# Kernel optimization log

Hardware: AMD Instinct MI355X
Metric: run time of the kernel (lower is better)

Reference implementation:

```python
import jax, jax.numpy as jnp
import numpy as np

N_TYPES = 4
N_RELS = 8
N, E, IN_DIM, OUT_DIM = 100000, 1600000, 64, 64
SQRT_DK = float(np.sqrt(OUT_DIM))  # num_heads = 1 -> d_k = out_dim


def setup_inputs() -> dict:
    key = jax.random.key(0)
    ks = jax.random.split(key, 12)
    s = 0.05  # keep activations well-scaled (xavier-ish)
    h = jax.random.normal(ks[0], (N, IN_DIM), jnp.float32)
    node_type = jax.random.randint(ks[1], (N,), 0, N_TYPES, jnp.int32)
    src = jax.random.randint(ks[2], (E,), 0, N, jnp.int32)
    dst = jax.random.randint(ks[3], (E,), 0, N, jnp.int32)
    etype = jax.random.randint(ks[4], (E,), 0, N_RELS, jnp.int32)
    k_lin = jax.random.normal(ks[5], (N_TYPES, IN_DIM, OUT_DIM), jnp.float32) * s
    q_lin = jax.random.normal(ks[6], (N_TYPES, IN_DIM, OUT_DIM), jnp.float32) * s
    v_lin = jax.random.normal(ks[7], (N_TYPES, IN_DIM, OUT_DIM), jnp.float32) * s
    a_lin = jax.random.normal(ks[8], (N_TYPES, OUT_DIM, OUT_DIM), jnp.float32) * s
    rel_att = jax.random.normal(ks[9], (N_RELS, OUT_DIM, OUT_DIM), jnp.float32) * s
    rel_msg = jax.random.normal(ks[10], (N_RELS, OUT_DIM, OUT_DIM), jnp.float32) * s
    rel_pri = jnp.ones((N_RELS,), jnp.float32)
    skip = jnp.ones((N_TYPES,), jnp.float32)
    return dict(h=h, node_type=node_type, src=src, dst=dst, etype=etype,
                k_lin=k_lin, q_lin=q_lin, v_lin=v_lin, a_lin=a_lin,
                rel_att=rel_att, rel_msg=rel_msg, rel_pri=rel_pri, skip=skip)


def _typed_matmul(x, W, node_type):
    # rgnn_relational_matmul_no_scatter_gather_list: per-node-type GEMM.
    # Small fixed loop over node types (4), masked accumulate.
    out = jnp.zeros((x.shape[0], W.shape[-1]), x.dtype)
    for t in range(W.shape[0]):
        out = out + jnp.where((node_type == t)[:, None], x @ W[t], 0.0)
    return out


def reference(h, node_type, src, dst, etype, k_lin, q_lin, v_lin, a_lin,
              rel_att, rel_msg, rel_pri, skip):
    # per-node-type K/Q/V projections (num_heads==1, d_k==out_dim)
    k = _typed_matmul(h, k_lin, node_type)  # [N, d_k]
    q = _typed_matmul(h, q_lin, node_type)  # [N, d_k]
    v = _typed_matmul(h, v_lin, node_type)  # [N, d_k]

    # q @ relation_att, computed per relation for ALL nodes then gathered per edge
    # (avoids materializing [E, d_k, d_k] relation weights per edge)
    qW = jnp.einsum('nd,rde->rne', q, rel_att)  # [R, N, d_k]
    t_edge = qW[etype, dst]                      # [E, d_k]  (dst-side product)
    # attention score: <q_dst @ W_att_r, k_src>
    score = jnp.sum(t_edge * k[src], axis=-1)    # [E]

    # edge softmax over incoming edges of each dst, scaled by pri/sqrt(d_k)
    logits = score * (rel_pri / SQRT_DK)[etype]
    m = jax.ops.segment_max(logits, dst, num_segments=N)
    ex = jnp.exp(logits - m[dst])
    den = jax.ops.segment_sum(ex, dst, num_segments=N)
    alpha = ex / jnp.where(den[dst] == 0, 1.0, den[dst])  # [E]

    # message: v_src @ W_msg_r, per relation then gathered per edge
    vW = jnp.einsum('nd,rde->rne', v, rel_msg)   # [R, N, d_k]
    msg = vW[etype, src]                          # [E, d_k]

    # softmax-weighted aggregation to dst nodes
    agg = jax.ops.segment_sum(alpha[:, None] * msg, dst, num_segments=N)  # [N, d_k]

    # output per-node-type GEMM with sigmoid(skip)-scaled a_linears
    W_out = jax.nn.sigmoid(skip)[:, None, None] * a_lin
    return _typed_matmul(agg, W_out, node_type)  # [N, out_dim]
```

## Files before the change

kernel.cpp:

```cpp
#include <hip/hip_runtime.h>
#include <math.h>

#define DIM 64
#define NT 4
#define NR 8

typedef __attribute__((ext_vector_type(8))) short bf16x8;
typedef __attribute__((ext_vector_type(8))) unsigned short u16x8;
typedef __attribute__((ext_vector_type(4))) float f32x4;

__device__ __forceinline__ unsigned short f2bf(float f) {
    unsigned u = __float_as_uint(f);
    return (unsigned short)((u + 0x7FFF + ((u >> 16) & 1)) >> 16);
}
__device__ __forceinline__ float bf2f(unsigned short u) {
    return __uint_as_float((unsigned)u << 16);
}
__device__ __forceinline__ bf16x8 ldb16(const unsigned short* p) {
    return *((const bf16x8*)p);
}

__global__ void prep_all(const float* __restrict__ A, const float* __restrict__ Mw,
                         const float* __restrict__ kl, const float* __restrict__ ql,
                         const float* __restrict__ vl,
                         unsigned short* __restrict__ At, unsigned short* __restrict__ Mt,
                         unsigned short* __restrict__ Wkt, unsigned short* __restrict__ Wqt,
                         unsigned short* __restrict__ Wvt,
                         int* __restrict__ cnt8, int* __restrict__ tm, int M) {
    int i = blockIdx.x * blockDim.x + threadIdx.x;
    if (i < M) cnt8[i] = 0;
    if (i < 16) tm[i] = 0;
    if (i >= 28 * DIM * DIM) return;
    int mat = i >> 12;
    int idx = i & 4095;
    int n = idx >> 6;
    int k = idx & 63;
    int so = k * DIM + n;
    if (mat < 8)       At [((size_t)mat << 12) + idx]        = f2bf(A [((size_t)mat << 12) + so]);
    else if (mat < 16) Mt [((size_t)(mat - 8) << 12) + idx]  = f2bf(Mw[((size_t)(mat - 8) << 12) + so]);
    else if (mat < 20) Wkt[((size_t)(mat - 16) << 12) + idx] = f2bf(kl[((size_t)(mat - 16) << 12) + so]);
    else if (mat < 24) Wqt[((size_t)(mat - 20) << 12) + idx] = f2bf(ql[((size_t)(mat - 20) << 12) + so]);
    else               Wvt[((size_t)(mat - 24) << 12) + idx] = f2bf(vl[((size_t)(mat - 24) << 12) + so]);
}

__global__ void type_count(const int* __restrict__ ntype, int* __restrict__ tm,
                           int* __restrict__ order, int N, int ocap) {
    int i = blockIdx.x * blockDim.x + threadIdx.x;
    if (i < ocap) order[i] = -1;
    int t = (i < N) ? ntype[i] : -1;
    int lane = threadIdx.x & 63;
    #pragma unroll
    for (int tt = 0; tt < NT; tt++) {
        unsigned long long m = __ballot(t == tt);
        int c = __popcll(m);
        if (c && lane == (__ffsll((long long)m) - 1)) atomicAdd(&tm[tt], c);
    }
}

__global__ void type_scan(int* __restrict__ tm) {
    if (threadIdx.x == 0 && blockIdx.x == 0) {
        int b = 0;
        for (int t = 0; t < NT; t++) { tm[4 + t] = b; b += ((tm[t] + 63) >> 6) << 6; }
        tm[12] = b;
    }
}

__global__ void type_scatter(const int* __restrict__ ntype, int* __restrict__ tm,
                             int* __restrict__ order, int N) {
    int i = blockIdx.x * blockDim.x + threadIdx.x;
    int t = (i < N) ? ntype[i] : -1;
    int lane = threadIdx.x & 63;
    #pragma unroll
    for (int tt = 0; tt < NT; tt++) {
        unsigned long long m = __ballot(t == tt);
        int c = __popcll(m);
        if (!c) continue;
        int ldr = __ffsll((long long)m) - 1;
        int base = 0;
        if (lane == ldr) base = atomicAdd(&tm[8 + tt], c);
        base = __shfl(base, ldr, 64);
        if (t == tt) {
            int rank = __popcll(m & ((1ull << lane) - 1ull));
            order[tm[4 + tt] + base + rank] = i;
        }
    }
}

__global__ void __launch_bounds__(256)
proj_mfma(const float* __restrict__ h, const int* __restrict__ ntype,
          const int* __restrict__ order, const int* __restrict__ tm,
          const unsigned short* __restrict__ Wkt, const unsigned short* __restrict__ Wqt,
          const unsigned short* __restrict__ Wvt,
          unsigned short* __restrict__ kvbf, unsigned short* __restrict__ qbf, int N) {
    __shared__ __align__(16) unsigned short xs[64][72];
    int t  = threadIdx.x;
    int n0 = blockIdx.x * 64;
    if (n0 >= tm[12]) return;
    int first = order[n0];
    if (first < 0) return;
    int ty = ntype[first];

    int grow[2];
    #pragma unroll
    for (int i = 0; i < 2; i++) grow[i] = order[n0 + (t + 256 * i) / 8];

    #pragma unroll
    for (int i = 0; i < 4; i++) {
        int idx = t + 256 * i;
        int row = idx >> 4, c4 = idx & 15;
        int gn = order[n0 + row];
        float4 xv = make_float4(0.f, 0.f, 0.f, 0.f);
        if (gn >= 0) xv = ((const float4*)(h + (size_t)gn * DIM))[c4];
        ushort4 b = make_ushort4(f2bf(xv.x), f2bf(xv.y), f2bf(xv.z), f2bf(xv.w));
        *((ushort4*)&xs[row][c4 * 4]) = b;
    }
    __syncthreads();

    int wave = t >> 6, lane = t & 63;
    int m = lane & 15, quad = lane >> 4;
    bf16x8 xa0 = *((const bf16x8*)&xs[wave * 16 + m][quad * 8]);
    bf16x8 xa1 = *((const bf16x8*)&xs[wave * 16 + m][32 + quad * 8]);

    const unsigned short* Wt[3] = { Wkt + (size_t)ty * 4096,
                                    Wqt + (size_t)ty * 4096,
                                    Wvt + (size_t)ty * 4096 };
    for (int mm = 0; mm < 3; mm++) {
        const unsigned short* W = Wt[mm];
        f32x4 c0 = {0.f,0.f,0.f,0.f}, c1 = c0, c2 = c0, c3 = c0;
        c0 = __builtin_amdgcn_mfma_f32_16x16x32_bf16(xa0, ldb16(W + (( 0 + m) << 6)      + quad * 8), c0, 0, 0, 0);
        c1 = __builtin_amdgcn_mfma_f32_16x16x32_bf16(xa0, ldb16(W + ((16 + m) << 6)      + quad * 8), c1, 0, 0, 0);
        c2 = __builtin_amdgcn_mfma_f32_16x16x32_bf16(xa0, ldb16(W + ((32 + m) << 6)      + quad * 8), c2, 0, 0, 0);
        c3 = __builtin_amdgcn_mfma_f32_16x16x32_bf16(xa0, ldb16(W + ((48 + m) << 6)      + quad * 8), c3, 0, 0, 0);
        c0 = __builtin_amdgcn_mfma_f32_16x16x32_bf16(xa1, ldb16(W + (( 0 + m) << 6) + 32 + quad * 8), c0, 0, 0, 0);
        c1 = __builtin_amdgcn_mfma_f32_16x16x32_bf16(xa1, ldb16(W + ((16 + m) << 6) + 32 + quad * 8), c1, 0, 0, 0);
        c2 = __builtin_amdgcn_mfma_f32_16x16x32_bf16(xa1, ldb16(W + ((32 + m) << 6) + 32 + quad * 8), c2, 0, 0, 0);
        c3 = __builtin_amdgcn_mfma_f32_16x16x32_bf16(xa1, ldb16(W + ((48 + m) << 6) + 32 + quad * 8), c3, 0, 0, 0);

        __syncthreads();
        #pragma unroll
        for (int reg = 0; reg < 4; reg++) {
            unsigned short* qr = &xs[wave * 16 + quad * 4 + reg][m];
            qr[ 0] = f2bf(c0[reg]); qr[16] = f2bf(c1[reg]);
            qr[32] = f2bf(c2[reg]); qr[48] = f2bf(c3[reg]);
        }
        __syncthreads();
        #pragma unroll
        for (int i = 0; i < 2; i++) {
            int idx = t + 256 * i;
            int row = idx >> 3, c8 = idx & 7;
            u16x8 v = *((const u16x8*)&xs[row][c8 * 8]);
            if (mm == 1) {
                *((u16x8*)(qbf + ((size_t)(n0 + row) << 6) + c8 * 8)) = v;
            } else {
                int gn = grow[i];
                if (gn >= 0) {
                    unsigned short* dp = (mm == 0)
                        ? kvbf + ((size_t)gn << 7) + c8 * 8
                        : kvbf + ((size_t)gn << 7) + 64 + c8 * 8;
                    *((u16x8*)dp) = v;
                }
            }
        }
    }
}

__global__ void hist8(const int* __restrict__ dst, const int* __restrict__ et,
                      int* __restrict__ cnt, int* __restrict__ rank, int E) {
    int e = blockIdx.x * blockDim.x + threadIdx.x;
    if (e < E) rank[e] = atomicAdd(&cnt[dst[e] * NR + et[e]], 1);
}

__global__ void scan1(const int* __restrict__ cnt, int* __restrict__ off,
                      int* __restrict__ bsum, int M) {
    __shared__ int wsum[16];
    int tid = threadIdx.x;
    int lane = tid & 63, wid = tid >> 6;
    int i = blockIdx.x * 1024 + tid;
    int x0 = (i < M) ? cnt[i] : 0;
    int x = x0;
    #pragma unroll
    for (int s = 1; s < 64; s <<= 1) {
        int y = __shfl_up(x, s, 64);
        if (lane >= s) x += y;
    }
    if (lane == 63) wsum[wid] = x;
    __syncthreads();
    if (tid < 16) {
        int w = wsum[tid];
        #pragma unroll
        for (int s = 1; s < 16; s <<= 1) {
            int y = __shfl_up(w, s, 16);
            if (tid >= s) w += y;
        }
        wsum[tid] = w;
    }
    __syncthreads();
    int add = (wid > 0) ? wsum[wid - 1] : 0;
    if (i < M) off[i] = add + x - x0;
    if (tid == 1023) bsum[blockIdx.x] = wsum[15];
}

__global__ void scan2(int* __restrict__ bsum, int nb) {
    __shared__ int wsum[16];
    __shared__ int carry;
    int tid = threadIdx.x;
    int lane = tid & 63, wid = tid >> 6;
    if (tid == 0) carry = 0;
    __syncthreads();
    for (int base = 0; base < nb; base += 1024) {
        int i = base + tid;
        int x0 = (i < nb) ? bsum[i] : 0;
        int x = x0;
        #pragma unroll
        for (int s = 1; s < 64; s <<= 1) {
            int y = __shfl_up(x, s, 64);
            if (lane >= s) x += y;
        }
        if (lane == 63) wsum[wid] = x;
        __syncthreads();
        if (tid < 16) {
            int w = wsum[tid];
            #pragma unroll
            for (int s = 1; s < 16; s <<= 1) {
                int y = __shfl_up(w, s, 16);
                if (tid >= s) w += y;
            }
            wsum[tid] = w;
        }
        __syncthreads();
        int add = carry + ((wid > 0) ? wsum[wid - 1] : 0);
        if (i < nb) bsum[i] = add + x - x0;
        __syncthreads();
        if (tid == 0) carry += wsum[15];
        __syncthreads();
    }
}

__global__ void scan3(int* __restrict__ off, const int* __restrict__ bsum, int M, int E) {
    int i = blockIdx.x * 1024 + threadIdx.x;
    if (i < M) off[i] += bsum[blockIdx.x];
    if (i == 0) off[M] = E;
}

__global__ void scatter8(const int* __restrict__ src, const int* __restrict__ dst,
                         const int* __restrict__ et, const int* __restrict__ off,
                         const int* __restrict__ rank, int* __restrict__ se, int E) {
    int e = blockIdx.x * blockDim.x + threadIdx.x;
    if (e >= E) return;
    int key = dst[e] * NR + et[e];
    se[off[key] + rank[e]] = src[e];
}

__global__ void __launch_bounds__(256)
fused_edge(const unsigned short* __restrict__ qbf,
           const unsigned short* __restrict__ kvbf,
           const unsigned short* __restrict__ At,
           const unsigned short* __restrict__ Mt,
           const int* __restrict__ se, const int* __restrict__ off8,
           const float* __restrict__ rel_pri,
           const int* __restrict__ ntype, const int* __restrict__ order,
           const int* __restrict__ tm,
           const float* __restrict__ Wa, const float* __restrict__ skip,
           float* __restrict__ out, int N) {
    __shared__ __align__(16) unsigned short smem[2][4][16][72];
    __shared__ __align__(16) float W2[64][64];
    unsigned short (*qwb)[16][72] = smem[0];
    unsigned short (*pl)[16][72]  = smem[1];
    const int t    = threadIdx.x;
    const int wave = t >> 6;
    const int lane = t & 63;
    const int m    = lane & 15;
    const int quad = lane >> 4;
    const int sg   = lane >> 2;
    const int ll   = lane & 3;
    const int n0   = blockIdx.x * 64 + wave * 16;
    const int tot  = tm[12];
    const bool blkvalid = (blockIdx.x * 64) < tot;

    if (blkvalid) {
        const int ty = ntype[order[blockIdx.x * 64]];
        const float sgs = 1.f / (1.f + expf(-skip[ty]));
        const float4* wg = (const float4*)(Wa + (size_t)ty * DIM * DIM);
        float4* wl = (float4*)&W2[0][0];
        #pragma unroll
        for (int i = 0; i < 4; i++) {
            float4 w = wg[t + 256 * i];
            w.x *= sgs; w.y *= sgs; w.z *= sgs; w.w *= sgs;
            wl[t + 256 * i] = w;
        }
    }
    __syncthreads();
    if (!blkvalid) return;

    const int nid = order[n0 + sg];
    const bool act = nid >= 0;
    const int nb8 = act ? nid * NR : 0;
    const int ovA = off8[nb8 + ll * 2];
    const int ovB = off8[nb8 + ll * 2 + 1];
    const int ovC = off8[nb8 + 8];

    const unsigned short* qp = qbf + ((size_t)(n0 + m) << 6) + quad * 8;
    const bf16x8 qa0 = *((const bf16x8*)qp);
    const bf16x8 qa1 = *((const bf16x8*)(qp + 32));

    f32x4 u0 = {0.f,0.f,0.f,0.f}, u1 = u0, u2 = u0, u3 = u0;
    float ddsum = 0.f;

    for (int r = 0; r < NR; r++) {
        const unsigned short* Ar = At + ((size_t)r << 12);
        f32x4 c0 = {0.f,0.f,0.f,0.f}, c1 = c0, c2 = c0, c3 = c0;
        c0 = __builtin_amdgcn_mfma_f32_16x16x32_bf16(qa0, ldb16(Ar + (( 0 + m) << 6)      + quad * 8), c0, 0, 0, 0);
        c1 = __builtin_amdgcn_mfma_f32_16x16x32_bf16(qa0, ldb16(Ar + ((16 + m) << 6)      + quad * 8), c1, 0, 0, 0);
        c2 = __builtin_amdgcn_mfma_f32_16x16x32_bf16(qa0, ldb16(Ar + ((32 + m) << 6)      + quad * 8), c2, 0, 0, 0);
        c3 = __builtin_amdgcn_mfma_f32_16x16x32_bf16(qa0, ldb16(Ar + ((48 + m) << 6)      + quad * 8), c3, 0, 0, 0);
        c0 = __builtin_amdgcn_mfma_f32_16x16x32_bf16(qa1, ldb16(Ar + (( 0 + m) << 6) + 32 + quad * 8), c0, 0, 0, 0);
        c1 = __builtin_amdgcn_mfma_f32_16x16x32_bf16(qa1, ldb16(Ar + ((16 + m) << 6) + 32 + quad * 8), c1, 0, 0, 0);
        c2 = __builtin_amdgcn_mfma_f32_16x16x32_bf16(qa1, ldb16(Ar + ((32 + m) << 6) + 32 + quad * 8), c2, 0, 0, 0);
        c3 = __builtin_amdgcn_mfma_f32_16x16x32_bf16(qa1, ldb16(Ar + ((48 + m) << 6) + 32 + quad * 8), c3, 0, 0, 0);

        #pragma unroll
        for (int reg = 0; reg < 4; reg++) {
            unsigned short* qr = &qwb[wave][quad * 4 + reg][m];
            qr[ 0] = f2bf(c0[reg]); qr[16] = f2bf(c1[reg]);
            qr[32] = f2bf(c2[reg]); qr[48] = f2bf(c3[reg]);
        }
        asm volatile("s_waitcnt lgkmcnt(0)" ::: "memory");

        const int bl0 = (sg << 2) | (r >> 1);
        const int va  = __shfl(ovA, bl0, 64);
        const int vb  = __shfl(ovB, bl0, 64);
        const int i0  = (r & 1) ? vb : va;
        const int rr  = r + 1;
        const int bl1 = ((sg << 2) | ((rr >> 1) & 3));
        const int wa2 = __shfl(ovA, bl1, 64);
        const int wb2 = __shfl(ovB, bl1, 64);
        int i1 = (rr == 8) ? ovC : ((rr & 1) ? wb2 : wa2);
        if (!act) i1 = i0;

        const float pri = rel_pri[r] * 0.125f;
        float P[16];
        #pragma unroll
        for (int x = 0; x < 16; x++) P[x] = 0.f;
        float dd = 0.f;

        if (i0 < i1) {
            const u16x8 tq0 = *((const u16x8*)&qwb[wave][sg][ll * 16]);
            const u16x8 tq1 = *((const u16x8*)&qwb[wave][sg][ll * 16 + 8]);
            float tq[16];
            #pragma unroll
            for (int x = 0; x < 8; x++) { tq[x] = bf2f(tq0[x]); tq[8 + x] = bf2f(tq1[x]); }

            for (int i = i0; i < i1; i += 2) {
                const int sA = se[i];
                const bool hB = (i + 1 < i1);
                const int sB = se[hB ? i + 1 : i];
                const unsigned short* pA = kvbf + ((size_t)sA << 7) + ll * 16;
                const unsigned short* pB = kvbf + ((size_t)sB << 7) + ll * 16;
                const u16x8 kA0 = *((const u16x8*)pA);
                const u16x8 kA1 = *((const u16x8*)(pA + 8));
                const u16x8 vA0 = *((const u16x8*)(pA + 64));
                const u16x8 vA1 = *((const u16x8*)(pA + 72));
                const u16x8 kB0 = *((const u16x8*)pB);
                const u16x8 kB1 = *((const u16x8*)(pB + 8));
                const u16x8 vB0 = *((const u16x8*)(pB + 64));
                const u16x8 vB1 = *((const u16x8*)(pB + 72));
                float sa = 0.f, sb = 0.f;
                #pragma unroll
                for (int x = 0; x < 8; x++) {
                    sa = fmaf(bf2f(kA0[x]), tq[x],     sa);
                    sa = fmaf(bf2f(kA1[x]), tq[8 + x], sa);
                    sb = fmaf(bf2f(kB0[x]), tq[x],     sb);
                    sb = fmaf(bf2f(kB1[x]), tq[8 + x], sb);
                }
                sa += __shfl_xor(sa, 1, 4);
                sa += __shfl_xor(sa, 2, 4);
                sb += __shfl_xor(sb, 1, 4);
                sb += __shfl_xor(sb, 2, 4);
                const float eA = __expf(sa * pri);
                const float eB = hB ? __expf(sb * pri) : 0.f;
                dd += eA + eB;
                #pragma unroll
                for (int x = 0; x < 8; x++) {
                    P[x]     = fmaf(eA, bf2f(vA0[x]), P[x]);
                    P[8 + x] = fmaf(eA, bf2f(vA1[x]), P[8 + x]);
                    P[x]     = fmaf(eB, bf2f(vB0[x]), P[x]);
                    P[8 + x] = fmaf(eB, bf2f(vB1[x]), P[8 + x]);
                }
            }
        }
        u16x8 w0, w1;
        #pragma unroll
        for (int x = 0; x < 8; x++) {
            w0[x] = f2bf(P[x]);
            w1[x] = f2bf(P[8 + x]);
        }
        *((u16x8*)&pl[wave][sg][ll * 16])     = w0;
        *((u16x8*)&pl[wave][sg][ll * 16 + 8]) = w1;
        ddsum += dd;
        asm volatile("s_waitcnt lgkmcnt(0)" ::: "memory");

        const unsigned short* Mr = Mt + ((size_t)r << 12);
        const bf16x8 pa0 = *((const bf16x8*)&pl[wave][m][quad * 8]);
        const bf16x8 pa1 = *((const bf16x8*)&pl[wave][m][32 + quad * 8]);
        u0 = __builtin_amdgcn_mfma_f32_16x16x32_bf16(pa0, ldb16(Mr + (( 0 + m) << 6)      + quad * 8), u0, 0, 0, 0);
        u1 = __builtin_amdgcn_mfma_f32_16x16x32_bf16(pa0, ldb16(Mr + ((16 + m) << 6)      + quad * 8), u1, 0, 0, 0);
        u2 = __builtin_amdgcn_mfma_f32_16x16x32_bf16(pa0, ldb16(Mr + ((32 + m) << 6)      + quad * 8), u2, 0, 0, 0);
        u3 = __builtin_amdgcn_mfma_f32_16x16x32_bf16(pa0, ldb16(Mr + ((48 + m) << 6)      + quad * 8), u3, 0, 0, 0);
        u0 = __builtin_amdgcn_mfma_f32_16x16x32_bf16(pa1, ldb16(Mr + (( 0 + m) << 6) + 32 + quad * 8), u0, 0, 0, 0);
        u1 = __builtin_amdgcn_mfma_f32_16x16x32_bf16(pa1, ldb16(Mr + ((16 + m) << 6) + 32 + quad * 8), u1, 0, 0, 0);
        u2 = __builtin_amdgcn_mfma_f32_16x16x32_bf16(pa1, ldb16(Mr + ((32 + m) << 6) + 32 + quad * 8), u2, 0, 0, 0);
        u3 = __builtin_amdgcn_mfma_f32_16x16x32_bf16(pa1, ldb16(Mr + ((48 + m) << 6) + 32 + quad * 8), u3, 0, 0, 0);
        asm volatile("s_waitcnt lgkmcnt(0)" ::: "memory");
    }

    __syncthreads();
    float* Ut = (float*)&smem[0][0][0][0];
    #pragma unroll
    for (int reg = 0; reg < 4; reg++) {
        const int row = quad * 4 + reg;
        const float dv  = __shfl(ddsum, row << 2, 64);
        const float inv = (dv == 0.f) ? 0.f : 1.f / dv;
        float* rp = Ut + ((size_t)(wave * 16 + row)) * 68 + m;
        rp[ 0] = u0[reg] * inv;
        rp[16] = u1[reg] * inv;
        rp[32] = u2[reg] * inv;
        rp[48] = u3[reg] * inv;
    }
    asm volatile("s_waitcnt lgkmcnt(0)" ::: "memory");

    const int og  = lane & 15;
    const int ng4 = (lane >> 4) * 4;
    float4 a0 = make_float4(0.f,0.f,0.f,0.f), a1 = a0, a2 = a0, a3 = a0;
    const float* xb = Ut + ((size_t)(wave * 16 + ng4)) * 68;
    #pragma unroll 8
    for (int d = 0; d < DIM; d++) {
        float4 wv = *((const float4*)&W2[d][og * 4]);
        float x0 = xb[d];
        float x1 = xb[68 + d];
        float x2 = xb[136 + d];
        float x3 = xb[204 + d];
        a0.x = fmaf(x0, wv.x, a0.x); a0.y = fmaf(x0, wv.y, a0.y);
        a0.z = fmaf(x0, wv.z, a0.z); a0.w = fmaf(x0, wv.w, a0.w);
        a1.x = fmaf(x1, wv.x, a1.x); a1.y = fmaf(x1, wv.y, a1.y);
        a1.z = fmaf(x1, wv.z, a1.z); a1.w = fmaf(x1, wv.w, a1.w);
        a2.x = fmaf(x2, wv.x, a2.x); a2.y = fmaf(x2, wv.y, a2.y);
        a2.z = fmaf(x2, wv.z, a2.z); a2.w = fmaf(x2, wv.w, a2.w);
        a3.x = fmaf(x3, wv.x, a3.x); a3.y = fmaf(x3, wv.y, a3.y);
        a3.z = fmaf(x3, wv.z, a3.z); a3.w = fmaf(x3, wv.w, a3.w);
    }
    const int g0 = order[n0 + ng4 + 0];
    const int g1 = order[n0 + ng4 + 1];
    const int g2 = order[n0 + ng4 + 2];
    const int g3 = order[n0 + ng4 + 3];
    if (g0 >= 0) ((float4*)(out + (size_t)g0 * DIM))[og] = a0;
    if (g1 >= 0) ((float4*)(out + (size_t)g1 * DIM))[og] = a1;
    if (g2 >= 0) ((float4*)(out + (size_t)g2 * DIM))[og] = a2;
    if (g3 >= 0) ((float4*)(out + (size_t)g3 * DIM))[og] = a3;
}

extern "C" void kernel_launch(void* const* d_in, const int* in_sizes, int n_in,
                              void* d_out, int out_size, void* d_ws, size_t ws_size,
                              hipStream_t stream) {
    const float* h       = (const float*)d_in[0];
    const int*   ntype   = (const int*)  d_in[1];
    const int*   src     = (const int*)  d_in[2];
    const int*   dst     = (const int*)  d_in[3];
    const int*   et      = (const int*)  d_in[4];
    const float* k_lin   = (const float*)d_in[5];
    const float* q_lin   = (const float*)d_in[6];
    const float* v_lin   = (const float*)d_in[7];
    const float* a_lin   = (const float*)d_in[8];
    const float* rel_att = (const float*)d_in[9];
    const float* rel_msg = (const float*)d_in[10];
    const float* rel_pri = (const float*)d_in[11];
    const float* skip    = (const float*)d_in[12];

    int N = in_sizes[1];
    int E = in_sizes[2];
    int M = N * NR;
    int ocap = N + NT * 64;

    float* ws = (float*)d_ws;
    size_t o = 0;
    unsigned short* kvbf = (unsigned short*)(ws + o); o += (size_t)N * DIM;
    unsigned short* qbf  = (unsigned short*)(ws + o); o += (size_t)ocap * DIM / 2;
    int* off8   = (int*)(ws + o); o += (size_t)M + 1024;
    int* cnt8   = (int*)(ws + o); o += (size_t)M;
    int* rank   = (int*)(ws + o); o += (size_t)E;
    int* se     = (int*)(ws + o); o += (size_t)E;
    int* bsum   = (int*)(ws + o); o += 1024;
    int* order  = (int*)(ws + o); o += (size_t)ocap;
    int* tm     = (int*)(ws + o); o += 16;
    unsigned short* At  = (unsigned short*)(ws + o); o += (size_t)NR * DIM * DIM / 2;
    unsigned short* Mt  = (unsigned short*)(ws + o); o += (size_t)NR * DIM * DIM / 2;
    unsigned short* Wkt = (unsigned short*)(ws + o); o += (size_t)NT * DIM * DIM / 2;
    unsigned short* Wqt = (unsigned short*)(ws + o); o += (size_t)NT * DIM * DIM / 2;
    unsigned short* Wvt = (unsigned short*)(ws + o); o += (size_t)NT * DIM * DIM / 2;

    float* out = (float*)d_out;

    int gprep = (M > 28 * DIM * DIM ? M : 28 * DIM * DIM);
    prep_all<<<(gprep + 255) / 256, 256, 0, stream>>>(
        rel_att, rel_msg, k_lin, q_lin, v_lin, At, Mt, Wkt, Wqt, Wvt, cnt8, tm, M);

    type_count<<<(ocap + 255) / 256, 256, 0, stream>>>(ntype, tm, order, N, ocap);
    type_scan<<<1, 64, 0, stream>>>(tm);
    type_scatter<<<(N + 255) / 256, 256, 0, stream>>>(ntype, tm, order, N);

    int gridT = (N + NT * 64 + 63) / 64;
    proj_mfma<<<gridT, 256, 0, stream>>>(h, ntype, order, tm, Wkt, Wqt, Wvt,
                                         kvbf, qbf, N);

    hist8<<<(E + 255) / 256, 256, 0, stream>>>(dst, et, cnt8, rank, E);
    int nb = (M + 1023) / 1024;
    scan1<<<nb, 1024, 0, stream>>>(cnt8, off8, bsum, M);
    scan2<<<1, 1024, 0, stream>>>(bsum, nb);
    scan3<<<nb, 1024, 0, stream>>>(off8, bsum, M, E);
    scatter8<<<(E + 255) / 256, 256, 0, stream>>>(src, dst, et, off8, rank, se, E);

    fused_edge<<<gridT, 256, 0, stream>>>(qbf, kvbf, At, Mt, se, off8, rel_pri,
                                          ntype, order, tm, a_lin, skip, out, N);
}
```

Baseline: 590.5 us.

## Key CSR edge buckets by type-sorted node position instead of node id

Adds a pos array mapping each node to its slot in the type-sorted order, and builds the dst×relation CSR offsets keyed by that sorted position. The fused edge kernel then reads a contiguous block of offsets per 64-node tile with coalesced loads instead of gathering per-node offsets through order[]. Edge lists for a tile become contiguous in se, which should improve locality. In exchange the histogram and scatter kernels take an extra indirection through pos, and the CSR arrays grow to cover padding slots.

```diff
diff --git a/kernel.cpp b/kernel.cpp
--- a/kernel.cpp
+++ b/kernel.cpp
@@ -26,9 +26,9 @@
                          unsigned short* __restrict__ At, unsigned short* __restrict__ Mt,
                          unsigned short* __restrict__ Wkt, unsigned short* __restrict__ Wqt,
                          unsigned short* __restrict__ Wvt,
-                         int* __restrict__ cnt8, int* __restrict__ tm, int M) {
+                         int* __restrict__ cnt8, int* __restrict__ tm, int M2) {
     int i = blockIdx.x * blockDim.x + threadIdx.x;
-    if (i < M) cnt8[i] = 0;
+    if (i < M2) cnt8[i] = 0;
     if (i < 16) tm[i] = 0;
     if (i >= 28 * DIM * DIM) return;
     int mat = i >> 12;
@@ -44,9 +44,9 @@
 }
 
 __global__ void type_count(const int* __restrict__ ntype, int* __restrict__ tm,
-                           int* __restrict__ order, int N, int ocap) {
+                           int* __restrict__ order, int N, int ocap2) {
     int i = blockIdx.x * blockDim.x + threadIdx.x;
-    if (i < ocap) order[i] = -1;
+    if (i < ocap2) order[i] = -1;
     int t = (i < N) ? ntype[i] : -1;
     int lane = threadIdx.x & 63;
     #pragma unroll
@@ -66,7 +66,7 @@
 }
 
 __global__ void type_scatter(const int* __restrict__ ntype, int* __restrict__ tm,
-                             int* __restrict__ order, int N) {
+                             int* __restrict__ order, int* __restrict__ pos, int N) {
     int i = blockIdx.x * blockDim.x + threadIdx.x;
     int t = (i < N) ? ntype[i] : -1;
     int lane = threadIdx.x & 63;
@@ -81,7 +81,9 @@
         base = __shfl(base, ldr, 64);
         if (t == tt) {
             int rank = __popcll(m & ((1ull << lane) - 1ull));
-            order[tm[4 + tt] + base + rank] = i;
+            int p = tm[4 + tt] + base + rank;
+            order[p] = i;
+            pos[i] = p;
         }
     }
 }
@@ -165,9 +167,10 @@
 }
 
 __global__ void hist8(const int* __restrict__ dst, const int* __restrict__ et,
+                      const int* __restrict__ pos,
                       int* __restrict__ cnt, int* __restrict__ rank, int E) {
     int e = blockIdx.x * blockDim.x + threadIdx.x;
-    if (e < E) rank[e] = atomicAdd(&cnt[dst[e] * NR + et[e]], 1);
+    if (e < E) rank[e] = atomicAdd(&cnt[pos[dst[e]] * NR + et[e]], 1);
 }
 
 __global__ void scan1(const int* __restrict__ cnt, int* __restrict__ off,
@@ -243,11 +246,12 @@
 }
 
 __global__ void scatter8(const int* __restrict__ src, const int* __restrict__ dst,
-                         const int* __restrict__ et, const int* __restrict__ off,
+                         const int* __restrict__ et, const int* __restrict__ pos,
+                         const int* __restrict__ off,
                          const int* __restrict__ rank, int* __restrict__ se, int E) {
     int e = blockIdx.x * blockDim.x + threadIdx.x;
     if (e >= E) return;
-    int key = dst[e] * NR + et[e];
+    int key = pos[dst[e]] * NR + et[e];
     se[off[key] + rank[e]] = src[e];
 }
 
@@ -292,12 +296,10 @@
     __syncthreads();
     if (!blkvalid) return;
 
-    const int nid = order[n0 + sg];
-    const bool act = nid >= 0;
-    const int nb8 = act ? nid * NR : 0;
-    const int ovA = off8[nb8 + ll * 2];
-    const int ovB = off8[nb8 + ll * 2 + 1];
-    const int ovC = off8[nb8 + 8];
+    const int ob  = n0 * NR;
+    const int ov0 = off8[ob + lane];
+    const int ov1 = off8[ob + 64 + lane];
+    const int ov2 = off8[ob + 128];
 
     const unsigned short* qp = qbf + ((size_t)(n0 + m) << 6) + quad * 8;
     const bf16x8 qa0 = *((const bf16x8*)qp);
@@ -326,16 +328,14 @@
         }
         asm volatile("s_waitcnt lgkmcnt(0)" ::: "memory");
 
-        const int bl0 = (sg << 2) | (r >> 1);
-        const int va  = __shfl(ovA, bl0, 64);
-        const int vb  = __shfl(ovB, bl0, 64);
-        const int i0  = (r & 1) ? vb : va;
-        const int rr  = r + 1;
-        const int bl1 = ((sg << 2) | ((rr >> 1) & 3));
-        const int wa2 = __shfl(ovA, bl1, 64);
-        const int wb2 = __shfl(ovB, bl1, 64);
-        int i1 = (rr == 8) ? ovC : ((rr & 1) ? wb2 : wa2);
-        if (!act) i1 = i0;
+        const int g  = sg * NR + r;
+        const int g1 = g + 1;
+        const int x0a = __shfl(ov0, g, 64);
+        const int x0b = __shfl(ov1, g - 64, 64);
+        const int i0  = (g < 64) ? x0a : x0b;
+        const int x1a = __shfl(ov0, g1, 64);
+        const int x1b = __shfl(ov1, g1 - 64, 64);
+        const int i1  = (g1 < 64) ? x1a : ((g1 < 128) ? x1b : ov2);
 
         const float pri = rel_pri[r] * 0.125f;
         float P[16];
@@ -477,19 +477,21 @@
 
     int N = in_sizes[1];
     int E = in_sizes[2];
-    int M = N * NR;
-    int ocap = N + NT * 64;
+    int gridT = (N + NT * 64 + 63) / 64;
+    int ocap2 = gridT * 64;
+    int M2 = ocap2 * NR;
 
     float* ws = (float*)d_ws;
     size_t o = 0;
     unsigned short* kvbf = (unsigned short*)(ws + o); o += (size_t)N * DIM;
-    unsigned short* qbf  = (unsigned short*)(ws + o); o += (size_t)ocap * DIM / 2;
-    int* off8   = (int*)(ws + o); o += (size_t)M + 1024;
-    int* cnt8   = (int*)(ws + o); o += (size_t)M;
+    unsigned short* qbf  = (unsigned short*)(ws + o); o += (size_t)ocap2 * DIM / 2;
+    int* off8   = (int*)(ws + o); o += (size_t)M2 + 1024;
+    int* cnt8   = (int*)(ws + o); o += (size_t)M2;
     int* rank   = (int*)(ws + o); o += (size_t)E;
     int* se     = (int*)(ws + o); o += (size_t)E;
     int* bsum   = (int*)(ws + o); o += 1024;
-    int* order  = (int*)(ws + o); o += (size_t)ocap;
+    int* order  = (int*)(ws + o); o += (size_t)ocap2;
+    int* pos    = (int*)(ws + o); o += (size_t)N;
     int* tm     = (int*)(ws + o); o += 16;
     unsigned short* At  = (unsigned short*)(ws + o); o += (size_t)NR * DIM * DIM / 2;
     unsigned short* Mt  = (unsigned short*)(ws + o); o += (size_t)NR * DIM * DIM / 2;
@@ -499,24 +501,23 @@
 
     float* out = (float*)d_out;
 
-    int gprep = (M > 28 * DIM * DIM ? M : 28 * DIM * DIM);
+    int gprep = (M2 > 28 * DIM * DIM ? M2 : 28 * DIM * DIM);
     prep_all<<<(gprep + 255) / 256, 256, 0, stream>>>(
-        rel_att, rel_msg, k_lin, q_lin, v_lin, At, Mt, Wkt, Wqt, Wvt, cnt8, tm, M);
-
-    type_count<<<(ocap + 255) / 256, 256, 0, stream>>>(ntype, tm, order, N, ocap);
+        rel_att, rel_msg, k_lin, q_lin, v_lin, At, Mt, Wkt, Wqt, Wvt, cnt8, tm, M2);
+
+    type_count<<<(ocap2 + 255) / 256, 256, 0, stream>>>(ntype, tm, order, N, ocap2);
     type_scan<<<1, 64, 0, stream>>>(tm);
-    type_scatter<<<(N + 255) / 256, 256, 0, stream>>>(ntype, tm, order, N);
-
-    int gridT = (N + NT * 64 + 63) / 64;
+    type_scatter<<<(N + 255) / 256, 256, 0, stream>>>(ntype, tm, order, pos, N);
+
     proj_mfma<<<gridT, 256, 0, stream>>>(h, ntype, order, tm, Wkt, Wqt, Wvt,
                                          kvbf, qbf, N);
 
-    hist8<<<(E + 255) / 256, 256, 0, stream>>>(dst, et, cnt8, rank, E);
-    int nb = (M + 1023) / 1024;
-    scan1<<<nb, 1024, 0, stream>>>(cnt8, off8, bsum, M);
+    hist8<<<(E + 255) / 256, 256, 0, stream>>>(dst, et, pos, cnt8, rank, E);
+    int nb = (M2 + 1023) / 1024;
+    scan1<<<nb, 1024, 0, stream>>>(cnt8, off8, bsum, M2);
     scan2<<<1, 1024, 0, stream>>>(bsum, nb);
-    scan3<<<nb, 1024, 0, stream>>>(off8, bsum, M, E);
-    scatter8<<<(E + 255) / 256, 256, 0, stream>>>(src, dst, et, off8, rank, se, E);
+    scan3<<<nb, 1024, 0, stream>>>(off8, bsum, M2, E);
+    scatter8<<<(E + 255) / 256, 256, 0, stream>>>(src, dst, et, pos, off8, rank, se, E);
 
     fused_edge<<<gridT, 256, 0, stream>>>(qbf, kvbf, At, Mt, se, off8, rel_pri,
                                           ntype, order, tm, a_lin, skip, out, N);
```

Measured after the change: 587.5 us. No clear change (-0.5%).
